# Optimization experiments

Hardware: AMD Instinct MI355X
Metric: run time of the kernel (lower is better)

The kernel has to match this reference:

```python
import jax, jax.numpy as jnp
import numpy as np

N_EXPERTS = 8
TOP_K = 2


def setup_inputs() -> dict:
    key = jax.random.key(0)
    k1, k2, k3, k4 = jax.random.split(key, 4)
    B, S, D, E = 8, 4096, 1024, N_EXPERTS
    x = jax.random.normal(k1, (B, S, D), dtype=jnp.float32)
    gate_w = jax.random.normal(k2, (D, E), dtype=jnp.float32) * (1.0 / np.sqrt(D))
    expert_w = jax.random.normal(k3, (E, D, D), dtype=jnp.float32) * (1.0 / np.sqrt(D))
    expert_b = jax.random.normal(k4, (E, D), dtype=jnp.float32) * 0.01
    return {"x": x, "gate_w": gate_w, "expert_w": expert_w, "expert_b": expert_b}


def reference(x, gate_w, expert_w, expert_b):
    B, S, D = x.shape
    E = expert_w.shape[0]
    xt = x.reshape(-1, D)                       # [T, D], T = B*S
    T = xt.shape[0]
    gate_logits = xt @ gate_w                   # [T, E]
    weights, selected = jax.lax.top_k(gate_logits, TOP_K)   # [T, K]
    weights = jax.nn.softmax(weights.astype(jnp.float32), axis=1).astype(x.dtype)
    # Per-token combine weights over experts (top-k indices are distinct -> scatter-add is exact)
    combine = jnp.zeros((T, E), dtype=x.dtype).at[jnp.arange(T)[:, None], selected].add(weights)  # [T, E]
    out = jnp.zeros_like(xt)
    for e in range(E):  # fixed small expert count, mirrors the module's expert loop
        out = out + combine[:, e:e + 1] * (xt @ expert_w[e] + expert_b[e])
    return out.reshape(x.shape)
```

## Files before the change

### kernel.cpp

```cpp
#include <hip/hip_runtime.h>
#include <hip/hip_bf16.h>


typedef __attribute__((ext_vector_type(8))) short short8_t;
typedef __attribute__((ext_vector_type(4))) float f32x4_t;
typedef __attribute__((ext_vector_type(4))) unsigned short us4_t;

#define GLOAD_LDS16(g, l)                                                                     \
  __builtin_amdgcn_global_load_lds((const __attribute__((address_space(1))) unsigned int*)(g), \
                                   (__attribute__((address_space(3))) unsigned int*)(l), 16, 0, 0)

__device__ __forceinline__ unsigned short f2bf(float f) {
  union { __hip_bfloat16 h; unsigned short u; } c;
  c.h = __float2bfloat16(f);
  return c.u;
}
__device__ __forceinline__ float bf2f(unsigned short u) {
  union { unsigned int i; float f; } c;
  c.i = ((unsigned int)u) << 16;
  return c.f;
}

__global__ __launch_bounds__(256) void gate_kernel(
    const float* __restrict__ x, const float* __restrict__ gw,
    unsigned short* __restrict__ xb,
    int* __restrict__ tok_e, float* __restrict__ tok_w)
{
  int wid = threadIdx.x >> 6, lane = threadIdx.x & 63;
  int t0 = (blockIdx.x << 4) + (wid << 2);
  const float4* g4 = (const float4*)gw;
  float lg[4][8] = {};
  #pragma unroll
  for (int c = 0; c < 4; ++c) {
    int d4 = (c << 6) + lane;
    float4 ga[4], gb[4];
    #pragma unroll
    for (int j = 0; j < 4; ++j) {
      int d = (d4 << 2) + j;
      ga[j] = g4[d << 1];
      gb[j] = g4[(d << 1) + 1];
    }
    #pragma unroll
    for (int t = 0; t < 4; ++t) {
      const float4* x4 = (const float4*)(x + ((size_t)(t0 + t) << 10));
      float4 v = x4[d4];
      unsigned long long pk = (unsigned long long)f2bf(v.x)
                            | ((unsigned long long)f2bf(v.y) << 16)
                            | ((unsigned long long)f2bf(v.z) << 32)
                            | ((unsigned long long)f2bf(v.w) << 48);
      ((unsigned long long*)(xb + ((size_t)(t0 + t) << 10)))[d4] = pk;
      float xs[4] = {v.x, v.y, v.z, v.w};
      #pragma unroll
      for (int j = 0; j < 4; ++j) {
        lg[t][0] += xs[j]*ga[j].x; lg[t][1] += xs[j]*ga[j].y;
        lg[t][2] += xs[j]*ga[j].z; lg[t][3] += xs[j]*ga[j].w;
        lg[t][4] += xs[j]*gb[j].x; lg[t][5] += xs[j]*gb[j].y;
        lg[t][6] += xs[j]*gb[j].z; lg[t][7] += xs[j]*gb[j].w;
      }
    }
  }
  #pragma unroll
  for (int t = 0; t < 4; ++t)
    #pragma unroll
    for (int e = 0; e < 8; ++e) {
      float v = lg[t][e];
      #pragma unroll
      for (int s = 32; s > 0; s >>= 1) v += __shfl_xor(v, s, 64);
      lg[t][e] = v;
    }
  if (lane < 4) {
    int t = t0 + lane;
    float m0 = lg[lane][0], m1 = -3.4e38f; int e0 = 0, e1 = 0;
    #pragma unroll
    for (int e = 1; e < 8; ++e) {
      float v = lg[lane][e];
      if (v > m0) { m1 = m0; e1 = e0; m0 = v; e0 = e; }
      else if (v > m1) { m1 = v; e1 = e; }
    }
    float p1 = 1.0f / (1.0f + expf(m0 - m1));
    float p0 = 1.0f - p1;
    int i0 = t << 1;
    tok_e[i0]   = e0; tok_w[i0]   = p0;
    tok_e[i0+1] = e1; tok_w[i0+1] = p1;
  }
}

__global__ __launch_bounds__(256) void hist_kernel(
    const int* __restrict__ tok_e, int* __restrict__ tok_r, int* __restrict__ chunkhist)
{
  __shared__ int lh[8];
  if (threadIdx.x < 8) lh[threadIdx.x] = 0;
  __syncthreads();
  int i = (blockIdx.x << 8) + threadIdx.x;
  int e = tok_e[i];
  tok_r[i] = atomicAdd(&lh[e], 1);
  __syncthreads();
  if (threadIdx.x < 8) chunkhist[(blockIdx.x << 3) + threadIdx.x] = lh[threadIdx.x];
}

__global__ __launch_bounds__(512) void scan_kernel(
    const int* __restrict__ chunkhist, int* __restrict__ base, int* __restrict__ ctrl)
{
  __shared__ int h[2048];
  __shared__ int bx[2048];
  __shared__ int tot[8], eoff[8];
  for (int i = threadIdx.x; i < 2048; i += 512) h[i] = chunkhist[i];
  __syncthreads();
  int wid = threadIdx.x >> 6, lane = threadIdx.x & 63;
  int running = 0;
  #pragma unroll
  for (int b = 0; b < 4; ++b) {
    int c = (b << 6) + lane;
    int orig = h[(c << 3) + wid];
    int v = orig;
    #pragma unroll
    for (int s = 1; s < 64; s <<= 1) {
      int u = __shfl_up(v, s, 64);
      if (lane >= s) v += u;
    }
    bx[(c << 3) + wid] = running + v - orig;
    running += __shfl(v, 63, 64);
  }
  if (lane == 0) tot[wid] = running;
  __syncthreads();
  if (threadIdx.x == 0) {
    int off = 0, boff = 0;
    #pragma unroll
    for (int e = 0; e < 8; ++e) {
      ctrl[e] = tot[e];
      ctrl[8 + e] = off; eoff[e] = off; off += tot[e];
      ctrl[16 + e] = boff; boff += (tot[e] + 127) >> 7;
    }
    ctrl[24] = boff;
  }
  __syncthreads();
  for (int i = threadIdx.x; i < 2048; i += 512) base[i] = bx[i] + eoff[i & 7];
}

__global__ __launch_bounds__(256) void scatter_kernel(
    const int* __restrict__ tok_e, const int* __restrict__ tok_r, const float* __restrict__ tok_w,
    const int* __restrict__ base, int* __restrict__ slot_token, float* __restrict__ slot_w)
{
  int i = (blockIdx.x << 8) + threadIdx.x;
  int e = tok_e[i];
  int slot = base[((i >> 8) << 3) + e] + tok_r[i];
  slot_token[slot] = (i >> 1) | ((i & 1) << 16);
  slot_w[slot] = tok_w[i];
}

__global__ __launch_bounds__(256) void wconv_kernel(const float* __restrict__ w,
                                                    unsigned short* __restrict__ wt)
{
  __shared__ float tile[32][33];
  const float* we = w + ((size_t)blockIdx.z << 20);
  unsigned short* wte = wt + ((size_t)blockIdx.z << 20);
  int k0 = blockIdx.x << 5, n0 = blockIdx.y << 5;
  for (int i = threadIdx.x; i < 1024; i += 256) {
    int k = i >> 5, n = i & 31;
    tile[k][n] = we[(size_t)(k0 + k) * 1024 + n0 + n];
  }
  __syncthreads();
  for (int i = threadIdx.x; i < 1024; i += 256) {
    int n = i >> 5, k = i & 31;
    wte[(size_t)(n0 + n) * 1024 + k0 + k] = f2bf(tile[k][n]);
  }
}

__global__ __launch_bounds__(256, 2) void moe_gemm(
    const unsigned short* __restrict__ xb, const unsigned short* __restrict__ wt,
    const float* __restrict__ bias, const int* __restrict__ ctrl,
    const int* __restrict__ slot_token, const float* __restrict__ slot_w,
    unsigned short* __restrict__ part, float* __restrict__ out, int total_slots, int use_part)
{
  __shared__ unsigned short Alds[3 * 128 * 32];
  __shared__ unsigned short Blds[3 * 256 * 32];
  __shared__ int   tokid[128];
  __shared__ int   kslot[128];
  __shared__ float wrow[128];

  int d = blockIdx.x;
  int xcd = d & 7, nb = (d >> 3) & 3, gbase = d >> 5;
  int by = (gbase << 3) | xcd;
  if (by >= ctrl[24]) return;
  int e = 0;
  #pragma unroll
  for (int i = 1; i < 8; ++i) if (by >= ctrl[16 + i]) e = i;
  int mblk = by - ctrl[16 + e];
  int cnt  = ctrl[e];
  int slot0 = ctrl[8 + e] + (mblk << 7);
  int rows_valid = cnt - (mblk << 7); if (rows_valid > 128) rows_valid = 128;

  int tid = threadIdx.x;
  if (tid < 128) {
    int s = slot0 + tid; if (s > total_slots - 1) s = total_slots - 1;
    int v = slot_token[s];
    tokid[tid] = v & 0xFFFF;
    kslot[tid] = v >> 16;
    wrow[tid]  = slot_w[s];
  }
  __syncthreads();

  int lane = tid & 63, w = tid >> 6;
  int wm = w >> 1, wn = w & 1;
  int l15 = lane & 15, hk = lane >> 4;
  int bn0 = nb << 8;
  const unsigned short* wte = wt + ((size_t)e << 20);

  int rr = tid >> 2;
  int kswz = (tid & 3) ^ ((tid >> 3) & 3);
  const unsigned short* gA0 = xb + ((size_t)tokid[rr] << 10) + (kswz << 3);
  const unsigned short* gA1 = xb + ((size_t)tokid[64 + rr] << 10) + (kswz << 3);
  const unsigned short* gB0 = wte + ((size_t)(bn0 + rr) << 10) + (kswz << 3);
  const unsigned short* gB1 = wte + ((size_t)(bn0 + 64 + rr) << 10) + (kswz << 3);
  const unsigned short* gB2 = wte + ((size_t)(bn0 + 128 + rr) << 10) + (kswz << 3);
  const unsigned short* gB3 = wte + ((size_t)(bn0 + 192 + rr) << 10) + (kswz << 3);
  int wbase = w << 9;

  f32x4_t acc[4][8] = {};

#define STAGE(NB, KO)                                                         \
  GLOAD_LDS16(gA0 + (KO), &Alds[(NB) * 4096 + wbase]);                        \
  GLOAD_LDS16(gA1 + (KO), &Alds[(NB) * 4096 + 2048 + wbase]);                 \
  GLOAD_LDS16(gB0 + (KO), &Blds[(NB) * 8192 + wbase]);                        \
  GLOAD_LDS16(gB1 + (KO), &Blds[(NB) * 8192 + 2048 + wbase]);                 \
  GLOAD_LDS16(gB2 + (KO), &Blds[(NB) * 8192 + 4096 + wbase]);                 \
  GLOAD_LDS16(gB3 + (KO), &Blds[(NB) * 8192 + 6144 + wbase]);

#define TILE(BUF, PF, NB2, KO2)                                               \
  { short8_t aF[4], bF[8];                                                    \
    _Pragma("unroll") for (int m = 0; m < 4; ++m) {                           \
      int ar = (wm << 6) + (m << 4) + l15;                                    \
      aF[m] = *(const short8_t*)&Alds[(BUF) * 4096 + (ar << 5) + ((hk ^ ((ar >> 1) & 3)) << 3)]; } \
    _Pragma("unroll") for (int n = 0; n < 8; ++n) {                           \
      int br = (wn << 7) + (n << 4) + l15;                                    \
      bF[n] = *(const short8_t*)&Blds[(BUF) * 8192 + (br << 5) + ((hk ^ ((br >> 1) & 3)) << 3)]; } \
    if (PF) { STAGE(NB2, KO2) }                                               \
    __builtin_amdgcn_s_setprio(1);                                            \
    _Pragma("unroll") for (int m = 0; m < 4; ++m)                             \
    _Pragma("unroll") for (int n = 0; n < 8; ++n)                             \
      acc[m][n] = __builtin_amdgcn_mfma_f32_16x16x32_bf16(aF[m], bF[n], acc[m][n], 0, 0, 0); \
    __builtin_amdgcn_s_setprio(0); }

#define VM6 asm volatile("s_waitcnt vmcnt(6)" ::: "memory");
#define BARR __builtin_amdgcn_s_barrier();

  STAGE(0, 0)
  STAGE(1, 32)
  VM6
  BARR
  for (int i = 0; i < 10; ++i) {
    int t = i * 3;
    TILE(0, 1, 2, (t + 2) << 5)
    VM6
    BARR
    TILE(1, 1, 0, (t + 3) << 5)
    VM6
    BARR
    TILE(2, 1, 1, (t + 4) << 5)
    VM6
    BARR
  }
  TILE(0, 0, 0, 0)
  asm volatile("s_waitcnt vmcnt(0)" ::: "memory");
  BARR
  TILE(1, 0, 0, 0)
#undef STAGE
#undef TILE
#undef VM6
#undef BARR

  const float* be = bias + (e << 10);
  float bv[8];
  #pragma unroll
  for (int nf = 0; nf < 8; ++nf) bv[nf] = be[bn0 + (wn << 7) + (nf << 4) + l15];
  #pragma unroll
  for (int mf = 0; mf < 4; ++mf) {
    int rbase = (wm << 6) + (mf << 4) + (hk << 2);
    #pragma unroll
    for (int r = 0; r < 4; ++r) {
      int row = rbase + r;
      if (row < rows_valid) {
        float wv = wrow[row];
        if (use_part) {
          size_t obase = ((size_t)((tokid[row] << 1) | kslot[row]) << 10);
          #pragma unroll
          for (int nf = 0; nf < 8; ++nf) {
            int dout = bn0 + (wn << 7) + (nf << 4) + l15;
            part[obase + dout] = f2bf(wv * (acc[mf][nf][r] + bv[nf]));
          }
        } else {
          size_t obase = ((size_t)tokid[row] << 10);
          #pragma unroll
          for (int nf = 0; nf < 8; ++nf) {
            int dout = bn0 + (wn << 7) + (nf << 4) + l15;
            atomicAdd(&out[obase + dout], wv * (acc[mf][nf][r] + bv[nf]));
          }
        }
      }
    }
  }
}

__global__ __launch_bounds__(256) void combine_kernel(
    const unsigned short* __restrict__ part, float* __restrict__ out)
{
  int t = blockIdx.x, i = threadIdx.x;
  const us4_t* p0 = (const us4_t*)(part + ((size_t)(t << 1) << 10));
  const us4_t* p1 = (const us4_t*)(part + ((size_t)((t << 1) | 1) << 10));
  us4_t a = p0[i], b = p1[i];
  float4 r;
  r.x = bf2f(a.x) + bf2f(b.x);
  r.y = bf2f(a.y) + bf2f(b.y);
  r.z = bf2f(a.z) + bf2f(b.z);
  r.w = bf2f(a.w) + bf2f(b.w);
  ((float4*)(out + ((size_t)t << 10)))[i] = r;
}

extern "C" void kernel_launch(void* const* d_in, const int* in_sizes, int n_in,
                              void* d_out, int out_size, void* d_ws, size_t ws_size,
                              hipStream_t stream) {
  (void)n_in;
  const float* x  = (const float*)d_in[0];
  const float* gw = (const float*)d_in[1];
  const float* ew = (const float*)d_in[2];
  const float* eb = (const float*)d_in[3];
  int T  = in_sizes[0] >> 10;
  int T2 = T << 1;

  char* wsb = (char*)d_ws;
  unsigned short* xb = (unsigned short*)wsb;
  size_t off = (size_t)T * 1024 * 2;
  unsigned short* wt = (unsigned short*)(wsb + off);
  off += (size_t)8 * 1024 * 1024 * 2;
  int* ctrl = (int*)(wsb + off); off += 256;
  int* tok_e = (int*)(wsb + off); off += (size_t)T2 * 4;
  int* tok_r = (int*)(wsb + off); off += (size_t)T2 * 4;
  float* tok_w = (float*)(wsb + off); off += (size_t)T2 * 4;
  int* slot_token = (int*)(wsb + off); off += (size_t)T2 * 4;
  float* slot_w = (float*)(wsb + off); off += (size_t)T2 * 4;
  int* chunkhist = (int*)(wsb + off); off += 2048 * 4;
  int* base = (int*)(wsb + off); off += 2048 * 4;
  unsigned short* part = (unsigned short*)(wsb + off);
  size_t need = off + (size_t)T2 * 1024 * 2;
  int use_part = (ws_size >= need) ? 1 : 0;

  float* out = (float*)d_out;

  if (!use_part)
    hipMemsetAsync(d_out, 0, (size_t)out_size * sizeof(float), stream);
  gate_kernel<<<T / 16, 256, 0, stream>>>(x, gw, xb, tok_e, tok_w);
  wconv_kernel<<<dim3(32, 32, 8), 256, 0, stream>>>(ew, wt);
  hist_kernel<<<T2 / 256, 256, 0, stream>>>(tok_e, tok_r, chunkhist);
  scan_kernel<<<1, 512, 0, stream>>>(chunkhist, base, ctrl);
  scatter_kernel<<<T2 / 256, 256, 0, stream>>>(tok_e, tok_r, tok_w, base,
                                               slot_token, slot_w);
  moe_gemm<<<2080, 256, 0, stream>>>(xb, wt, eb, ctrl, slot_token, slot_w,
                                     part, out, T2, use_part);
  if (use_part)
    combine_kernel<<<T, 256, 0, stream>>>(part, out);
}
```

Baseline: 304.6 us.

## Merge gate/wconv kernels and fuse routing into one cooperative kernel

Folds the weight conversion into the gating kernel's grid as extra blocks, and replaces the separate hist, scan and scatter kernels with a single cooperative kernel that uses grid-wide syncs. The combine kernel now uses a grid-stride loop over 4096 blocks. The aim is to cut kernel launch count and the gaps between small dependent kernels. In exchange it relies on cooperative-launch grid.sync, and the scan now runs on 256 threads instead of 512.

Result: slower. 360.4 us (+18.3%).

```diff
diff --git a/kernel.cpp b/kernel.cpp
--- a/kernel.cpp
+++ b/kernel.cpp
@@ -1,6 +1,9 @@
 #include <hip/hip_runtime.h>
 #include <hip/hip_bf16.h>
-
+#include <hip/hip_cooperative_groups.h>
+
+
+namespace cg = cooperative_groups;
 
 typedef __attribute__((ext_vector_type(8))) short short8_t;
 typedef __attribute__((ext_vector_type(4))) float f32x4_t;
@@ -21,11 +24,30 @@
   return c.f;
 }
 
-__global__ __launch_bounds__(256) void gate_kernel(
+__global__ __launch_bounds__(256) void gate_wconv_kernel(
     const float* __restrict__ x, const float* __restrict__ gw,
     unsigned short* __restrict__ xb,
-    int* __restrict__ tok_e, float* __restrict__ tok_w)
+    int* __restrict__ tok_e, float* __restrict__ tok_w,
+    const float* __restrict__ ew, unsigned short* __restrict__ wt)
 {
+  __shared__ float tile[32][33];
+  if (blockIdx.x >= 2048) {
+    int b = blockIdx.x - 2048;
+    int ez = b >> 10, rem = b & 1023;
+    int k0 = (rem & 31) << 5, n0 = (rem >> 5) << 5;
+    const float* we = ew + ((size_t)ez << 20);
+    unsigned short* wte = wt + ((size_t)ez << 20);
+    for (int i = threadIdx.x; i < 1024; i += 256) {
+      int k = i >> 5, n = i & 31;
+      tile[k][n] = we[(size_t)(k0 + k) * 1024 + n0 + n];
+    }
+    __syncthreads();
+    for (int i = threadIdx.x; i < 1024; i += 256) {
+      int n = i >> 5, k = i & 31;
+      wte[(size_t)(n0 + n) * 1024 + k0 + k] = f2bf(tile[k][n]);
+    }
+    return;
+  }
   int wid = threadIdx.x >> 6, lane = threadIdx.x & 63;
   int t0 = (blockIdx.x << 4) + (wid << 2);
   const float4* g4 = (const float4*)gw;
@@ -85,85 +107,65 @@
   }
 }
 
-__global__ __launch_bounds__(256) void hist_kernel(
-    const int* __restrict__ tok_e, int* __restrict__ tok_r, int* __restrict__ chunkhist)
+__global__ __launch_bounds__(256) void routing_kernel(
+    const int* __restrict__ tok_e, const float* __restrict__ tok_w,
+    int* __restrict__ chunkhist, int* __restrict__ base, int* __restrict__ ctrl,
+    int* __restrict__ slot_token, float* __restrict__ slot_w)
 {
+  cg::grid_group grid = cg::this_grid();
   __shared__ int lh[8];
+  __shared__ int bscan[2048];
+  __shared__ int tot[8], eoff[8];
+
   if (threadIdx.x < 8) lh[threadIdx.x] = 0;
   __syncthreads();
   int i = (blockIdx.x << 8) + threadIdx.x;
   int e = tok_e[i];
-  tok_r[i] = atomicAdd(&lh[e], 1);
+  int r = atomicAdd(&lh[e], 1);
   __syncthreads();
   if (threadIdx.x < 8) chunkhist[(blockIdx.x << 3) + threadIdx.x] = lh[threadIdx.x];
-}
-
-__global__ __launch_bounds__(512) void scan_kernel(
-    const int* __restrict__ chunkhist, int* __restrict__ base, int* __restrict__ ctrl)
-{
-  __shared__ int h[2048];
-  __shared__ int bx[2048];
-  __shared__ int tot[8], eoff[8];
-  for (int i = threadIdx.x; i < 2048; i += 512) h[i] = chunkhist[i];
-  __syncthreads();
-  int wid = threadIdx.x >> 6, lane = threadIdx.x & 63;
-  int running = 0;
-  #pragma unroll
-  for (int b = 0; b < 4; ++b) {
-    int c = (b << 6) + lane;
-    int orig = h[(c << 3) + wid];
-    int v = orig;
-    #pragma unroll
-    for (int s = 1; s < 64; s <<= 1) {
-      int u = __shfl_up(v, s, 64);
-      if (lane >= s) v += u;
-    }
-    bx[(c << 3) + wid] = running + v - orig;
-    running += __shfl(v, 63, 64);
-  }
-  if (lane == 0) tot[wid] = running;
-  __syncthreads();
-  if (threadIdx.x == 0) {
-    int off = 0, boff = 0;
-    #pragma unroll
-    for (int e = 0; e < 8; ++e) {
-      ctrl[e] = tot[e];
-      ctrl[8 + e] = off; eoff[e] = off; off += tot[e];
-      ctrl[16 + e] = boff; boff += (tot[e] + 127) >> 7;
-    }
-    ctrl[24] = boff;
-  }
-  __syncthreads();
-  for (int i = threadIdx.x; i < 2048; i += 512) base[i] = bx[i] + eoff[i & 7];
-}
-
-__global__ __launch_bounds__(256) void scatter_kernel(
-    const int* __restrict__ tok_e, const int* __restrict__ tok_r, const float* __restrict__ tok_w,
-    const int* __restrict__ base, int* __restrict__ slot_token, float* __restrict__ slot_w)
-{
-  int i = (blockIdx.x << 8) + threadIdx.x;
-  int e = tok_e[i];
-  int slot = base[((i >> 8) << 3) + e] + tok_r[i];
+  grid.sync();
+
+  if (blockIdx.x == 0) {
+    int wid = threadIdx.x >> 6, lane = threadIdx.x & 63;
+    #pragma unroll
+    for (int half = 0; half < 2; ++half) {
+      int ee = wid + (half << 2);
+      int running = 0;
+      #pragma unroll
+      for (int b = 0; b < 4; ++b) {
+        int c = (b << 6) + lane;
+        int orig = chunkhist[(c << 3) + ee];
+        int v = orig;
+        #pragma unroll
+        for (int s = 1; s < 64; s <<= 1) {
+          int u = __shfl_up(v, s, 64);
+          if (lane >= s) v += u;
+        }
+        bscan[(c << 3) + ee] = running + v - orig;
+        running += __shfl(v, 63, 64);
+      }
+      if (lane == 0) tot[ee] = running;
+    }
+    __syncthreads();
+    if (threadIdx.x == 0) {
+      int off = 0, boff = 0;
+      #pragma unroll
+      for (int ee = 0; ee < 8; ++ee) {
+        ctrl[ee] = tot[ee];
+        ctrl[8 + ee] = off; eoff[ee] = off; off += tot[ee];
+        ctrl[16 + ee] = boff; boff += (tot[ee] + 127) >> 7;
+      }
+      ctrl[24] = boff;
+    }
+    __syncthreads();
+    for (int j = threadIdx.x; j < 2048; j += 256) base[j] = bscan[j] + eoff[j & 7];
+  }
+  grid.sync();
+
+  int slot = base[(blockIdx.x << 3) + e] + r;
   slot_token[slot] = (i >> 1) | ((i & 1) << 16);
   slot_w[slot] = tok_w[i];
-}
-
-__global__ __launch_bounds__(256) void wconv_kernel(const float* __restrict__ w,
-                                                    unsigned short* __restrict__ wt)
-{
-  __shared__ float tile[32][33];
-  const float* we = w + ((size_t)blockIdx.z << 20);
-  unsigned short* wte = wt + ((size_t)blockIdx.z << 20);
-  int k0 = blockIdx.x << 5, n0 = blockIdx.y << 5;
-  for (int i = threadIdx.x; i < 1024; i += 256) {
-    int k = i >> 5, n = i & 31;
-    tile[k][n] = we[(size_t)(k0 + k) * 1024 + n0 + n];
-  }
-  __syncthreads();
-  for (int i = threadIdx.x; i < 1024; i += 256) {
-    int n = i >> 5, k = i & 31;
-    wte[(size_t)(n0 + n) * 1024 + k0 + k] = f2bf(tile[k][n]);
-  }
 }
 
 __global__ __launch_bounds__(256, 2) void moe_gemm(
@@ -302,18 +304,20 @@
 }
 
 __global__ __launch_bounds__(256) void combine_kernel(
-    const unsigned short* __restrict__ part, float* __restrict__ out)
+    const unsigned short* __restrict__ part, float* __restrict__ out, int T)
 {
-  int t = blockIdx.x, i = threadIdx.x;
-  const us4_t* p0 = (const us4_t*)(part + ((size_t)(t << 1) << 10));
-  const us4_t* p1 = (const us4_t*)(part + ((size_t)((t << 1) | 1) << 10));
-  us4_t a = p0[i], b = p1[i];
-  float4 r;
-  r.x = bf2f(a.x) + bf2f(b.x);
-  r.y = bf2f(a.y) + bf2f(b.y);
-  r.z = bf2f(a.z) + bf2f(b.z);
-  r.w = bf2f(a.w) + bf2f(b.w);
-  ((float4*)(out + ((size_t)t << 10)))[i] = r;
+  for (int t = blockIdx.x; t < T; t += 4096) {
+    int i = threadIdx.x;
+    const us4_t* p0 = (const us4_t*)(part + ((size_t)(t << 1) << 10));
+    const us4_t* p1 = (const us4_t*)(part + ((size_t)((t << 1) | 1) << 10));
+    us4_t a = p0[i], b = p1[i];
+    float4 r;
+    r.x = bf2f(a.x) + bf2f(b.x);
+    r.y = bf2f(a.y) + bf2f(b.y);
+    r.z = bf2f(a.z) + bf2f(b.z);
+    r.w = bf2f(a.w) + bf2f(b.w);
+    ((float4*)(out + ((size_t)t << 10)))[i] = r;
+  }
 }
 
 extern "C" void kernel_launch(void* const* d_in, const int* in_sizes, int n_in,
@@ -334,7 +338,6 @@
   off += (size_t)8 * 1024 * 1024 * 2;
   int* ctrl = (int*)(wsb + off); off += 256;
   int* tok_e = (int*)(wsb + off); off += (size_t)T2 * 4;
-  int* tok_r = (int*)(wsb + off); off += (size_t)T2 * 4;
   float* tok_w = (float*)(wsb + off); off += (size_t)T2 * 4;
   int* slot_token = (int*)(wsb + off); off += (size_t)T2 * 4;
   float* slot_w = (float*)(wsb + off); off += (size_t)T2 * 4;
@@ -348,14 +351,19 @@
 
   if (!use_part)
     hipMemsetAsync(d_out, 0, (size_t)out_size * sizeof(float), stream);
-  gate_kernel<<<T / 16, 256, 0, stream>>>(x, gw, xb, tok_e, tok_w);
-  wconv_kernel<<<dim3(32, 32, 8), 256, 0, stream>>>(ew, wt);
-  hist_kernel<<<T2 / 256, 256, 0, stream>>>(tok_e, tok_r, chunkhist);
-  scan_kernel<<<1, 512, 0, stream>>>(chunkhist, base, ctrl);
-  scatter_kernel<<<T2 / 256, 256, 0, stream>>>(tok_e, tok_r, tok_w, base,
-                                               slot_token, slot_w);
+
+  gate_wconv_kernel<<<10240, 256, 0, stream>>>(x, gw, xb, tok_e, tok_w, ew, wt);
+
+  {
+    void* args[] = {(void*)&tok_e, (void*)&tok_w, (void*)&chunkhist, (void*)&base,
+                    (void*)&ctrl, (void*)&slot_token, (void*)&slot_w};
+    hipLaunchCooperativeKernel((void*)routing_kernel, dim3(256), dim3(256),
+                               args, 0, stream);
+  }
+
   moe_gemm<<<2080, 256, 0, stream>>>(xb, wt, eb, ctrl, slot_token, slot_w,
                                      part, out, T2, use_part);
+
   if (use_part)
-    combine_kernel<<<T, 256, 0, stream>>>(part, out);
-}
+    combine_kernel<<<4096, 256, 0, stream>>>(part, out, T);
+}
```
